# Kernel tuning notes

Hardware: AMD Instinct MI355X
Metric: run time of the kernel (lower is better)

## Reference

```python
import jax, jax.numpy as jnp
import numpy as np

NUM_WIRES = 12
NUM_LAYERS = 4
NUM_OUTPUTS = 4
BATCH = 1024
DIM = 2 ** NUM_WIRES


def _apply_1q(psi, U, w):
    # psi: (B, 2**n) complex64; U: (2,2) shared or (B,2,2) per-sample; wire 0 = most significant.
    B = psi.shape[0]
    L = 2 ** w
    R = DIM // (2 * L)
    psi = psi.reshape(B, L, 2, R)
    if U.ndim == 2:
        psi = jnp.einsum('ij,bljr->blir', U, psi)
    else:
        psi = jnp.einsum('bij,bljr->blir', U, psi)
    return psi.reshape(B, DIM)


def _cnot(psi, c, t):
    # CNOT(control=c, target=t): flip target amplitudes in the control=1 half.
    B = psi.shape[0]
    psi = psi.reshape((B,) + (2,) * NUM_WIRES)
    a0 = jax.lax.index_in_dim(psi, 0, c + 1, keepdims=True)
    a1 = jax.lax.index_in_dim(psi, 1, c + 1, keepdims=True)
    a1 = jnp.flip(a1, axis=t + 1)
    psi = jnp.concatenate([a0, a1], axis=c + 1)
    return psi.reshape(B, DIM)


def _rot(phi, theta, omega):
    # PennyLane Rot(phi, theta, omega) = RZ(omega) @ RY(theta) @ RZ(phi)
    c = jnp.cos(theta / 2)
    s = jnp.sin(theta / 2)
    u00 = jnp.exp(-0.5j * (phi + omega)) * c
    u01 = -jnp.exp(0.5j * (phi - omega)) * s
    u10 = jnp.exp(-0.5j * (phi - omega)) * s
    u11 = jnp.exp(0.5j * (phi + omega)) * c
    return jnp.stack([jnp.stack([u00, u01]), jnp.stack([u10, u11])]).astype(jnp.complex64)


def _circuit(inputs, weights):
    B = inputs.shape[0]
    psi = jnp.zeros((B, DIM), jnp.complex64).at[:, 0].set(1.0)
    # AngleEmbedding with rotation 'Y': RY(pi/2 * x_w) on wire w (per-sample angles)
    theta = (jnp.pi / 2) * inputs  # (B, n)
    c = jnp.cos(theta / 2)
    s = jnp.sin(theta / 2)
    for w in range(NUM_WIRES):
        U = jnp.stack([jnp.stack([c[:, w], -s[:, w]], -1),
                       jnp.stack([s[:, w], c[:, w]], -1)], -2).astype(jnp.complex64)  # (B,2,2)
        psi = _apply_1q(psi, U, w)
    # StronglyEntanglingLayers: Rot on every wire, then ring of CNOTs with range r
    for l in range(NUM_LAYERS):
        for w in range(NUM_WIRES):
            psi = _apply_1q(psi, _rot(weights[l, w, 0], weights[l, w, 1], weights[l, w, 2]), w)
        r = (l % (NUM_WIRES - 1)) + 1
        for w in range(NUM_WIRES):
            psi = _cnot(psi, w, (w + r) % NUM_WIRES)
    # expval(PauliZ) on the first NUM_OUTPUTS wires
    probs = jnp.abs(psi) ** 2  # (B, DIM) float32
    idx = jnp.arange(DIM)
    shifts = NUM_WIRES - 1 - jnp.arange(NUM_OUTPUTS)
    signs = (1.0 - 2.0 * ((idx[None, :] >> shifts[:, None]) & 1)).astype(probs.dtype)  # (NOUT, DIM)
    return probs @ signs.T  # (B, NUM_OUTPUTS)


def setup_inputs() -> dict:
    key = jax.random.key(0)
    k1, k2 = jax.random.split(key)
    inputs = jax.random.uniform(k1, (BATCH, NUM_WIRES), jnp.float32, -1.0, 1.0)
    weights = jax.random.uniform(k2, (NUM_LAYERS, NUM_WIRES, 3), jnp.float32, 0.0, 2.0 * np.pi)
    return {"inputs": inputs, "weights": weights}


def reference(inputs, weights):
    return _circuit(inputs, weights)
```

## Files before the change

### kernel.cpp

```cpp
#include <hip/hip_runtime.h>
#include <hip/hip_bf16.h>

#define NW 12
#define DIM 4096
#define NL 4
#define NGATE 48
#define NOUT 4
#define TPB 256

typedef float f32x2 __attribute__((ext_vector_type(2)));
typedef float f32x4 __attribute__((ext_vector_type(4)));
typedef unsigned u32x4 __attribute__((ext_vector_type(4)));
typedef short short8 __attribute__((ext_vector_type(8)));

constexpr int pcnt(unsigned x){ return __builtin_popcount(x); }
constexpr int msbp(unsigned x){ return x ? 31-__builtin_clz(x) : -1; }
constexpr unsigned ring_fwd(unsigned x,int r){
  for(int w=0;w<NW;++w){ int c=NW-1-w,t=NW-1-((w+r)%NW); x^=((x>>c)&1u)<<t; } return x;
}
constexpr unsigned ring_rev(unsigned x,int r){
  for(int w=NW-1;w>=0;--w){ int c=NW-1-w,t=NW-1-((w+r)%NW); x^=((x>>c)&1u)<<t; } return x;
}
struct Mat { unsigned col[12]; };
constexpr unsigned apply_cols(const Mat&M, unsigned v){
  unsigned r=0; for(int j=0;j<12;++j) if((v>>j)&1u) r^=M.col[j]; return r;
}
constexpr unsigned apply_rows(const unsigned* rows, unsigned v){
  unsigned r=0; for(int i=0;i<12;++i) r|=(unsigned)(pcnt(rows[i]&v)&1)<<i; return r;
}
constexpr bool invert_rows(const Mat&M, unsigned* ri_out){
  unsigned rb[12]={}, ri[12]={};
  for(int i=0;i<12;++i){ unsigned r=0; for(int j=0;j<12;++j) r|=((M.col[j]>>i)&1u)<<j; rb[i]=r; ri[i]=1u<<i; }
  for(int c=0;c<12;++c){
    int piv=-1; for(int r=c;r<12;++r) if((rb[r]>>c)&1u){piv=r;break;}
    if(piv<0) return false;
    unsigned t=rb[c]; rb[c]=rb[piv]; rb[piv]=t; t=ri[c]; ri[c]=ri[piv]; ri[piv]=t;
    for(int r=0;r<12;++r) if(r!=c&&((rb[r]>>c)&1u)){ rb[r]^=rb[c]; ri[r]^=ri[c]; }
  }
  for(int i=0;i<12;++i) ri_out[i]=ri[i];
  return true;
}
constexpr int nullspace4(const unsigned* A0, unsigned* out){
  unsigned A[4]={}; for(int i=0;i<4;++i) A[i]=A0[i];
  int rank=0; int pivc[4]={-1,-1,-1,-1};
  for(int c=0;c<12&&rank<4;++c){
    int piv=-1; for(int r=rank;r<4;++r) if((A[r]>>c)&1u){piv=r;break;}
    if(piv<0) continue;
    unsigned t=A[rank];A[rank]=A[piv];A[piv]=t;
    for(int r=0;r<4;++r) if(r!=rank&&((A[r]>>c)&1u)) A[r]^=A[rank];
    pivc[rank]=c; ++rank;
  }
  if(rank!=4) return -1;
  bool ispiv[12]={};
  for(int r=0;r<4;++r) ispiv[pivc[r]]=true;
  int cnt=0;
  for(int f=0;f<12;++f) if(!ispiv[f]){
    unsigned v=1u<<f;
    for(int r=0;r<4;++r) if((A[r]>>f)&1u) v|=1u<<pivc[r];
    out[cnt++]=v;
  }
  return cnt;
}
struct Ech { unsigned r[12]; int lead[12]; int n; };
constexpr unsigned ech_red(const Ech&e, unsigned v){
  int mv=msbp(v);
  for(int i=0;i<e.n&&v;++i) if(e.lead[i]==mv){ v^=e.r[i]; mv=msbp(v); }
  return v;
}
constexpr void ech_add(Ech&e, unsigned v){
  int l=msbp(v); int pos=e.n;
  while(pos>0&&e.lead[pos-1]<l){ e.r[pos]=e.r[pos-1]; e.lead[pos]=e.lead[pos-1]; --pos; }
  e.r[pos]=v; e.lead[pos]=l; e.n+=1;
}

struct Circ {
  unsigned M[NL][12]; unsigned RM[NL][12]; unsigned MR[NOUT];
};
constexpr Circ make_circ(){
  Circ C{};
  unsigned cols[12]={}, icols[12]={};
  for(int p=0;p<12;++p){ cols[p]=1u<<p; icols[p]=1u<<p; }
  for(int l=0;l<NL;++l){
    for(int w=0;w<NW;++w){
      int p=NW-1-w;
      C.M[l][w]=icols[p];
      unsigned r=0; for(int j=0;j<12;++j) r|=((cols[j]>>p)&1u)<<j;
      C.RM[l][w]=r;
    }
    int rr=(l%(NW-1))+1;
    for(int j=0;j<12;++j) cols[j]=ring_fwd(cols[j],rr);
    unsigned nic[12]={};
    for(int p=0;p<12;++p){
      unsigned y=ring_rev(1u<<p,rr), v=0;
      for(int q=0;q<12;++q) if((y>>q)&1u) v^=icols[q];
      nic[p]=v;
    }
    for(int p=0;p<12;++p) icols[p]=nic[p];
  }
  for(int o=0;o<NOUT;++o){
    int p=NW-1-o; unsigned r=0;
    for(int j=0;j<12;++j) r|=((cols[j]>>p)&1u)<<j;
    C.MR[o]=r;
  }
  return C;
}


constexpr unsigned amap(unsigned v){ return (v>>8)*2048u + (v&255u)*8u; }

struct Plan2 {
  unsigned SCOLt[8];
  unsigned SK16[16];
  unsigned TM;
  unsigned WBC[12][8], WOFF[12][16];
  unsigned RBC[12][8], ROFF[12][16];
  unsigned SRt[NOUT], KP[NOUT];
  bool ok;
};

constexpr Plan2 make_plan2(){
  Plan2 P{}; P.ok=true;
  constexpr Circ C = make_circ();
  const int SIGl[8] = {0,1,2,3,10,11,6,7};
  Mat Bprev{}; for(int j=0;j<12;++j) Bprev.col[j]=1u<<j;
  for(int g=0; g<12; ++g){
    int l=g/3, j0=(g%3)*4;
    unsigned mi[4]={}, rmi[4]={};
    for(int i=0;i<4;++i){ mi[i]=C.M[l][j0+i]; rmi[i]=C.RM[l][j0+i]; }
    unsigned u[8]={};
    if(nullspace4(rmi,u)!=8){ P.ok=false; return P; }
    unsigned binv[12]={};
    if(!invert_rows(Bprev,binv)){ P.ok=false; return P; }
    for(int s=0;s<8;++s) u[s]=apply_rows(binv,u[s]);
    Mat Bg{};
    for(int j=0;j<8;++j) Bg.col[j]=apply_cols(Bprev,u[j]);
    for(int i=0;i<4;++i) Bg.col[8+i]=mi[i];
    unsigned tinv[12]={};
    if(!invert_rows(Bg,tinv)){ P.ok=false; return P; }
    for(int i=0;i<4;++i)
      for(int j=0;j<12;++j){
        int want=(j==8+i)?1:0;
        if((pcnt(Bg.col[j]&rmi[i])&1)!=want){ P.ok=false; return P; }
      }
    if(g==0){
      for(int j=0;j<8;++j) P.SCOLt[j]=Bg.col[SIGl[j]];
      for(int idx=0;idx<16;++idx){
        unsigned v=0;
        if((idx>>2)&1) v^=Bg.col[4];
        if((idx>>2)&2) v^=Bg.col[5];
        if(idx&1) v^=Bg.col[8];
        if(idx&2) v^=Bg.col[9];
        P.SK16[idx]=v; P.TM|=v;
      }
    } else {
      unsigned rk[4]={};
      for(int i=0;i<4;++i){
        rk[i]=apply_rows(binv,mi[i]);
        if(apply_cols(Bprev,rk[i])!=mi[i]){ P.ok=false; return P; }
      }
      unsigned s2b[6]={u[0],u[1],u[2],u[3],rk[2],rk[3]};
      unsigned rows[12]={}; int nr=0;
      Ech P1{},P2{},ER{};
      for(int pick=0;pick<4;++pick){
        unsigned fx=0, fy=0;
        const int b1s[6]={0,1,2,3,10,11};
        for(int ii=0;ii<6;++ii){
          unsigned f=1u<<b1s[ii];
          unsigned p1=(f&15u)|(((f>>10)&3u)<<4);
          if(ech_red(P1,p1)){ fx=f; break; }
        }
        for(int bb=0;bb<12;++bb){
          unsigned f=1u<<bb, p2=0;
          for(int i2=0;i2<6;++i2) p2|=(unsigned)(pcnt(f&s2b[i2])&1)<<i2;
          if(ech_red(P2,p2)){ fy=f; break; }
        }
        if(!fx||!fy){ P.ok=false; return P; }
        unsigned cand[3]={fx,fy,fx^fy};
        unsigned chosen=0, cp1=0, cp2=0;
        for(int ci=0; ci<3 && !chosen; ++ci){
          unsigned f=cand[ci];
          unsigned p1=(f&15u)|(((f>>10)&3u)<<4);
          unsigned p2=0; for(int i2=0;i2<6;++i2) p2|=(unsigned)(pcnt(f&s2b[i2])&1)<<i2;
          if(ech_red(P1,p1)&&ech_red(P2,p2)){ chosen=f; cp1=p1; cp2=p2; }
        }
        if(!chosen){ P.ok=false; return P; }
        { unsigned v1=ech_red(P1,cp1); ech_add(P1,v1); }
        { unsigned v2=ech_red(P2,cp2); ech_add(P2,v2); }
        { unsigned vr=ech_red(ER,chosen); if(!vr){ P.ok=false; return P; } ech_add(ER,vr); }
        rows[nr++]=chosen;
      }
      for(int bb=0;bb<12 && nr<12;++bb){
        unsigned vr=ech_red(ER,1u<<bb); if(!vr) continue;
        ech_add(ER,vr); rows[nr++]=1u<<bb;
      }
      if(nr!=12){ P.ok=false; return P; }
      unsigned PhiCol[12]={};
      for(int j=0;j<12;++j){
        unsigned v=0;
        for(int i=0;i<12;++i) v|=(unsigned)((rows[i]>>j)&1u)<<i;
        PhiCol[j]=v;
      }
      unsigned PhiM[12]={};
      for(int j=0;j<12;++j){
        unsigned src=(j<8)? u[j] : rk[j-8];
        unsigned v=0;
        for(int q2=0;q2<12;++q2) if((src>>q2)&1u) v^=PhiCol[q2];
        PhiM[j]=v;
      }
      for(int j=0;j<8;++j){
        P.WBC[g][j]=amap(PhiCol[SIGl[j]]);
        P.RBC[g][j]=amap(PhiM[SIGl[j]]);
      }
      for(int idx=0;idx<16;++idx){
        unsigned wv=0, rv=0;
        if((idx>>2)&1){ wv^=PhiCol[4]; rv^=PhiM[4]; }
        if((idx>>2)&2){ wv^=PhiCol[5]; rv^=PhiM[5]; }
        if(idx&1){ wv^=PhiCol[8]; rv^=PhiM[8]; }
        if(idx&2){ wv^=PhiCol[9]; rv^=PhiM[9]; }
        P.WOFF[g][idx]=amap(wv); P.ROFF[g][idx]=amap(rv);
      }
    }
    Bprev=Bg;
  }
  for(int o=0;o<NOUT;++o){
    unsigned sr=0;
    for(int j=0;j<12;++j) sr|=(unsigned)(pcnt(Bprev.col[j]&C.MR[o])&1)<<j;
    unsigned srt=0;
    const int SIGl2[8] = {0,1,2,3,10,11,6,7};
    for(int j=0;j<8;++j) srt|=((sr>>SIGl2[j])&1u)<<j;
    P.SRt[o]=srt;
    unsigned kp=0;
    for(int idx=0;idx<16;++idx){
      int T=idx>>2, q=idx&3;
      unsigned bit=(((sr>>4)&1u)&(unsigned)(T&1))^(((sr>>5)&1u)&(unsigned)((T>>1)&1))
                  ^(((sr>>8)&1u)&(unsigned)(q&1))^(((sr>>9)&1u)&(unsigned)((q>>1)&1));
      kp|=bit<<idx;
    }
    P.KP[o]=kp;
  }
  return P;
}

constexpr Plan2 PL2C = make_plan2();
static_assert(PL2C.ok, "plan2 failed");
__device__ constexpr Plan2 PL2 = PL2C;

struct Plan {
  unsigned SCOL0[8]; unsigned SK16_0[16];
  unsigned WTC[12][8]; unsigned WK16[12][16];
  unsigned RDC[12][8]; unsigned WRK16[12][16];
  unsigned SRlow[NOUT], SRhigh[NOUT];
  unsigned TM; bool ok;
};
constexpr Plan make_plan(){
  Plan P{}; P.ok=true;
  constexpr Circ C = make_circ();
  Mat Bprev{}; for(int j=0;j<12;++j) Bprev.col[j]=1u<<j;
  for(int g=0; g<12; ++g){
    int l=g/3, j0=(g%3)*4;
    unsigned mi[4]={}, rmi[4]={};
    for(int i=0;i<4;++i){ mi[i]=C.M[l][j0+i]; rmi[i]=C.RM[l][j0+i]; }
    unsigned u[8]={};
    if(nullspace4(rmi,u)!=8){ P.ok=false; return P; }
    unsigned binv[12]={};
    if(!invert_rows(Bprev,binv)){ P.ok=false; return P; }
    for(int s=0;s<8;++s) u[s]=apply_rows(binv,u[s]);
    Mat Bg{};
    for(int j=0;j<8;++j) Bg.col[j]=apply_cols(Bprev,u[j]);
    for(int i=0;i<4;++i) Bg.col[8+i]=mi[i];
    unsigned tinv[12]={};
    if(!invert_rows(Bg,tinv)){ P.ok=false; return P; }
    for(int i=0;i<4;++i)
      for(int j=0;j<12;++j){
        int want=(j==8+i)?1:0;
        if((pcnt(Bg.col[j]&rmi[i])&1)!=want){ P.ok=false; return P; }
      }
    if(g==0){
      for(int j=0;j<8;++j) P.SCOL0[j]=Bg.col[j];
      unsigned tm=0;
      for(int k=0;k<16;++k){
        unsigned v=0; for(int i=0;i<4;++i) if((k>>i)&1) v^=Bg.col[8+i];
        P.SK16_0[k]=v; tm|=v;
      }
      P.TM=tm;
    } else {
      unsigned rk[4]={};
      for(int i=0;i<4;++i){
        rk[i]=apply_rows(binv,mi[i]);
        if(apply_cols(Bprev,rk[i])!=mi[i]){ P.ok=false; return P; }
      }
      unsigned row2[12]={};
      for(int bb=0;bb<12;++bb){
        unsigned r=0;
        for(int j=0;j<6;++j) r |= ((u[j]>>bb)&1u) << j;
        row2[bb]=r;
      }
      unsigned rows[12]={}; int nr=0;
      Ech P1{}; Ech P2{}; Ech ER{};
      for(int pick=0;pick<4;++pick){
        int b1=-1;
        for(int bb=0;bb<6;++bb){ if(ech_red(P1, 1u<<bb)){ b1=bb; break; } }
        int b2=-1;
        for(int bb=0;bb<12;++bb){ if(ech_red(P2, row2[bb])){ b2=bb; break; } }
        if(b1<0||b2<0){ P.ok=false; return P; }
        unsigned p2x=row2[b1];
        unsigned p1y=(b2<6)?(1u<<b2):0u;
        unsigned f=0, p1f=0, p2f=0;
        if(ech_red(P2,p2x))      { f=1u<<b1;            p1f=1u<<b1;          p2f=p2x; }
        else if(ech_red(P1,p1y)) { f=1u<<b2;            p1f=p1y;             p2f=row2[b2]; }
        else                     { f=(1u<<b1)^(1u<<b2); p1f=(1u<<b1)^p1y;    p2f=p2x^row2[b2]; }
        unsigned v1=ech_red(P1,p1f), v2=ech_red(P2,p2f);
        if(!v1||!v2){ P.ok=false; return P; }
        ech_add(P1,v1); ech_add(P2,v2);
        unsigned vr=ech_red(ER,f);
        if(!vr){ P.ok=false; return P; }
        ech_add(ER,vr);
        rows[nr++]=f;
      }
      for(int bb=0;bb<12 && nr<12;++bb){
        unsigned vr=ech_red(ER,1u<<bb); if(!vr) continue;
        ech_add(ER,vr); rows[nr++]=1u<<bb;
      }
      if(nr!=12){ P.ok=false; return P; }
      unsigned Wcol[12]={};
      for(int j=0;j<12;++j){
        unsigned v=0;
        for(int i=0;i<12;++i) v |= ((rows[i]>>j)&1u)<<i;
        Wcol[j]=v;
      }
      for(int j=0;j<8;++j){
        P.WTC[g][j]=Wcol[j];
        unsigned v=0;
        for(int q=0;q<12;++q) if((u[j]>>q)&1u) v^=Wcol[q];
        P.RDC[g][j]=v;
      }
      for(int k=0;k<16;++k){
        unsigned wv=0, rv=0;
        for(int i=0;i<4;++i) if((k>>i)&1){
          wv ^= Wcol[8+i];
          unsigned v=0;
          for(int q=0;q<12;++q) if((rk[i]>>q)&1u) v^=Wcol[q];
          rv ^= v;
        }
        P.WK16[g][k]=wv; P.WRK16[g][k]=rv;
      }
    }
    Bprev=Bg;
  }
  for(int o=0;o<NOUT;++o){
    unsigned sr=0;
    for(int j=0;j<12;++j) sr|=(unsigned)(pcnt(Bprev.col[j]&C.MR[o])&1)<<j;
    P.SRlow[o]=sr&255u; P.SRhigh[o]=sr>>8;
  }
  return P;
}
constexpr Plan PLC = make_plan();
static_assert(PLC.ok, "plan1 failed");
__device__ constexpr Plan PL = PLC;

__device__ __forceinline__ void gate_coeffs(const float* __restrict__ wts, int gi, float* o){
  const float* w = wts + gi*3;
  float st,ct;  sincosf(0.5f*w[1],&st,&ct);
  float sap,cap; sincosf(0.5f*(w[0]+w[2]),&sap,&cap);
  float sam,cam; sincosf(0.5f*(w[0]-w[2]),&sam,&cam);
  o[0]= cap*ct; o[1]=-sap*ct;
  o[2]=-cam*st; o[3]=-sam*st;
  o[4]= cam*st; o[5]=-sam*st;
  o[6]= cap*ct; o[7]= sap*ct;
}
__device__ __forceinline__ unsigned cvtpk(float a, float b){
  unsigned r; asm("v_cvt_pk_bf16_f32 %0, %1, %2" : "=v"(r) : "v"(a), "v"(b)); return r;
}
__device__ __forceinline__ void split2(float x, float& hf, float& lf){
  __hip_bfloat16 hb = __float2bfloat16(x);
  hf = __bfloat162float(hb);
  lf = x - hf;
}

__global__ void coeff2_kernel(const float* __restrict__ wts, unsigned short* __restrict__ gfrag){
  const int g = blockIdx.x;
  const int tid = threadIdx.x;
  const int m = tid & 15, rp = tid >> 4;
  const int s = rp >> 1, reg = rp & 1;
  const int r0 = 4*s + 2*reg, r1 = r0 + 1;
  const int l = g/3, j0 = (g%3)*4;
  float ur0=1.f, ui0=0.f, ur1=1.f, ui1=0.f;
  #pragma unroll
  for(int i=0;i<4;++i){
    float o[8]; gate_coeffs(wts, l*NW + j0 + i, o);
    int mb=(m>>i)&1, rb0=(r0>>i)&1, rb1=(r1>>i)&1;
    float er=o[(mb*2+rb0)*2], ei=o[(mb*2+rb0)*2+1];
    float tr=ur0*er-ui0*ei, ti=ur0*ei+ui0*er; ur0=tr; ui0=ti;
    er=o[(mb*2+rb1)*2]; ei=o[(mb*2+rb1)*2+1];
    tr=ur1*er-ui1*ei; ti=ur1*ei+ui1*er; ur1=tr; ui1=ti;
  }
  float ur0h,ur0l,ur1h,ur1l, ui0h,ui0l,ui1h,ui1l;
  split2(ur0,ur0h,ur0l); split2(ur1,ur1h,ur1l);
  split2(ui0,ui0h,ui0l); split2(ui1,ui1h,ui1l);
  unsigned Urh=cvtpk(ur0h,ur1h), Url=cvtpk(ur0l,ur1l);
  unsigned Uih=cvtpk(ui0h,ui1h), Uil=cvtpk(ui0l,ui1l);
  unsigned nUih=Uih^0x80008000u, nUil=Uil^0x80008000u;
  const int lane = s*16 + m;
  unsigned p0[6]={Urh,Url,Uih,Uil,nUih,nUil};
  unsigned p1[6]={Url,Urh,Uil,Uih,nUil,nUih};
  #pragma unroll
  for(int f=0; f<6; ++f){
    unsigned* fp = (unsigned*)((char*)gfrag + ((size_t)((g*6+f)*64 + lane))*16);
    fp[reg] = p0[f];
    fp[2+reg] = p1[f];
  }
}

__global__ __launch_bounds__(TPB,4)
void vqc_mfma(const float* __restrict__ inp, const unsigned short* __restrict__ gfrag,
              float* __restrict__ out){
  __shared__ __align__(16) char smem[DIM*8];
  float* cs = (float*)smem; float* ss = cs+NW; float* red = cs+2*NW;
  char* ampc = smem;
  const int t = threadIdx.x, b = blockIdx.x, l = t&63;
  if(t < NW){
    float x = inp[b*NW+t];
    float s,c; sincosf(0.78539816339744830962f*x,&s,&c);
    cs[t]=c; ss[t]=s;
  }
  __syncthreads();
  float ctm[12], stm[12];
  #pragma unroll
  for(int p=0;p<12;++p){ ctm[p]=cs[11-p]; stm[p]=ss[11-p]; }
  unsigned sigb=0;
  #pragma unroll
  for(int j=0;j<8;++j) sigb ^= ((t>>j)&1u)? PL2.SCOLt[j] : 0u;
  float pbase=1.f;
  #pragma unroll
  for(int p=0;p<12;++p)
    if(!((PL2C.TM>>p)&1u))
      pbase *= ((sigb>>p)&1u)? stm[p] : ctm[p];

  f32x4 Cr[4], Ci[4];
  #pragma unroll 1
  for(int g=0; g<12; ++g){
    if(g>0){
      unsigned wbase=0;
      #pragma unroll
      for(int j=0;j<8;++j) wbase ^= ((t>>j)&1u)? PL2.WBC[g][j] : 0u;
      __syncthreads();
      #pragma unroll
      for(int idx=0; idx<16; ++idx){
        const int T=idx>>2, q=idx&3;
        *(float2*)(ampc + (wbase ^ PL2.WOFF[g][idx])) = make_float2(Cr[T][q], Ci[T][q]);
      }
      __syncthreads();
    }
    short8 AF[6];
    #pragma unroll
    for(int f=0; f<6; ++f)
      AF[f] = *(const short8*)((const char*)gfrag + ((size_t)((g*6+f)*64 + l))*16);
    unsigned rbase=0;
    if(g>0){
      #pragma unroll
      for(int j=0;j<8;++j) rbase ^= ((t>>j)&1u)? PL2.RBC[g][j] : 0u;
    }
    #pragma unroll
    for(int T=0;T<4;++T){
      float2 v0,v1,v2,v3;
      if(g==0){
        float vv[4];
        #pragma unroll
        for(int rq=0;rq<4;++rq){
          unsigned sig = sigb ^ PL2.SK16[T*4+rq];
          float pk=pbase;
          #pragma unroll
          for(int p=0;p<12;++p)
            if((PL2C.TM>>p)&1u)
              pk *= ((sig>>p)&1u)? stm[p] : ctm[p];
          vv[rq]=pk;
        }
        v0=make_float2(vv[0],0.f); v1=make_float2(vv[1],0.f);
        v2=make_float2(vv[2],0.f); v3=make_float2(vv[3],0.f);
      } else {
        v0 = *(const float2*)(ampc + (rbase ^ PL2.ROFF[g][T*4+0]));
        v1 = *(const float2*)(ampc + (rbase ^ PL2.ROFF[g][T*4+1]));
        v2 = *(const float2*)(ampc + (rbase ^ PL2.ROFF[g][T*4+2]));
        v3 = *(const float2*)(ampc + (rbase ^ PL2.ROFF[g][T*4+3]));
      }
      float h0,h1,h2,h3,e0,e1,e2,e3;
      split2(v0.x,h0,e0); split2(v1.x,h1,e1); split2(v2.x,h2,e2); split2(v3.x,h3,e3);
      u32x4 bu; bu.x=cvtpk(h0,h1); bu.y=cvtpk(h2,h3); bu.z=cvtpk(e0,e1); bu.w=cvtpk(e2,e3);
      short8 Br = __builtin_bit_cast(short8, bu);
      split2(v0.y,h0,e0); split2(v1.y,h1,e1); split2(v2.y,h2,e2); split2(v3.y,h3,e3);
      u32x4 cu; cu.x=cvtpk(h0,h1); cu.y=cvtpk(h2,h3); cu.z=cvtpk(e0,e1); cu.w=cvtpk(e2,e3);
      short8 Bi = __builtin_bit_cast(short8, cu);
      const f32x4 z = {0.f,0.f,0.f,0.f};
      f32x4 cr = __builtin_amdgcn_mfma_f32_16x16x32_bf16(AF[0], Br, z, 0,0,0);
      cr = __builtin_amdgcn_mfma_f32_16x16x32_bf16(AF[1], Br, cr, 0,0,0);
      cr = __builtin_amdgcn_mfma_f32_16x16x32_bf16(AF[4], Bi, cr, 0,0,0);
      cr = __builtin_amdgcn_mfma_f32_16x16x32_bf16(AF[5], Bi, cr, 0,0,0);
      f32x4 ci = __builtin_amdgcn_mfma_f32_16x16x32_bf16(AF[2], Br, z, 0,0,0);
      ci = __builtin_amdgcn_mfma_f32_16x16x32_bf16(AF[3], Br, ci, 0,0,0);
      ci = __builtin_amdgcn_mfma_f32_16x16x32_bf16(AF[0], Bi, ci, 0,0,0);
      ci = __builtin_amdgcn_mfma_f32_16x16x32_bf16(AF[1], Bi, ci, 0,0,0);
      Cr[T]=cr; Ci[T]=ci;
    }
  }
  float acc[NOUT]={0.f,0.f,0.f,0.f};
  float sg[NOUT];
  #pragma unroll
  for(int o=0;o<NOUT;++o)
    sg[o] = (__popc((unsigned)t & PL2.SRt[o])&1)? -1.f : 1.f;
  #pragma unroll
  for(int idx=0; idx<16; ++idx){
    const int T=idx>>2, q=idx&3;
    float pr = Cr[T][q]*Cr[T][q] + Ci[T][q]*Ci[T][q];
    #pragma unroll
    for(int o=0;o<NOUT;++o){
      const bool kp = (PL2C.KP[o]>>idx)&1;
      float f = sg[o]*pr;
      acc[o] += kp? -f : f;
    }
  }
  #pragma unroll
  for(int o=0;o<NOUT;++o)
    #pragma unroll
    for(int off=32; off>0; off>>=1)
      acc[o] += __shfl_down(acc[o], off);
  __syncthreads();
  const int wv=t>>6, ln=t&63;
  if(ln==0){
    #pragma unroll
    for(int o=0;o<NOUT;++o) red[wv*NOUT+o]=acc[o];
  }
  __syncthreads();
  if(t<NOUT)
    out[b*NOUT+t] = red[0*NOUT+t]+red[1*NOUT+t]+red[2*NOUT+t]+red[3*NOUT+t];
}

__global__ __launch_bounds__(TPB,4)
void vqc_fb(const float* __restrict__ inp, const float* __restrict__ wts,
            float* __restrict__ out){
  __shared__ __align__(16) char smem[DIM*8 + NGATE*8*4];
  f32x2* amp = (f32x2*)smem;
  float* cs  = (float*)smem;
  float* ss  = cs + NW;
  float* red = cs + 2*NW;
  float* gtab = (float*)(smem + DIM*8);
  const int t = threadIdx.x;
  const int b = blockIdx.x;
  if(t < NW){
    float x = inp[b*NW+t];
    float s,c; sincosf(0.78539816339744830962f*x,&s,&c);
    cs[t]=c; ss[t]=s;
  }
  if(t < NGATE){
    float o[8]; gate_coeffs(wts,t,o);
    #pragma unroll
    for(int j=0;j<8;++j) gtab[t*8+j]=o[j];
  }
  __syncthreads();
  float cr[NW], sr_[NW];
  #pragma unroll
  for(int w=0;w<NW;++w){ cr[w]=cs[w]; sr_[w]=ss[w]; }
  unsigned sig_t=0;
  #pragma unroll
  for(int j=0;j<8;++j) sig_t ^= ((t>>j)&1u)? PL.SCOL0[j] : 0u;
  float pbase=1.f;
  #pragma unroll
  for(int p=0;p<12;++p)
    if(!((PLC.TM>>p)&1u))
      pbase *= ((sig_t>>p)&1u)? sr_[11-p] : cr[11-p];
  f32x2 a[16];
  #pragma unroll
  for(int k=0;k<16;++k){
    float pk=pbase;
    #pragma unroll
    for(int p=0;p<12;++p)
      if((PLC.TM>>p)&1u){
        unsigned bit = ((sig_t ^ PL.SK16_0[k])>>p)&1u;
        pk *= bit? sr_[11-p] : cr[11-p];
      }
    a[k].x=pk; a[k].y=0.f;
  }
  const float* gw = (const float*)gtab;
  #pragma unroll 1
  for(int g=0; g<12; ++g){
    if(g>0){
      unsigned wb=0, rb=0;
      #pragma unroll
      for(int j=0;j<8;++j){
        wb ^= ((t>>j)&1u)? PL.WTC[g][j] : 0u;
        rb ^= ((t>>j)&1u)? PL.RDC[g][j] : 0u;
      }
      __syncthreads();
      #pragma unroll
      for(int k=0;k<16;++k) amp[wb ^ PL.WK16[g][k]] = a[k];
      __syncthreads();
      #pragma unroll
      for(int k=0;k<16;++k) a[k] = amp[rb ^ PL.WRK16[g][k]];
    }
    #pragma unroll
    for(int i=0;i<4;++i){
      const float* w = gw + (g*4+i)*8;
      f32x2 c00={w[0],w[0]}, d00={-w[1],w[1]};
      f32x2 c01={w[2],w[2]}, d01={-w[3],w[3]};
      f32x2 c10={w[4],w[4]}, d10={-w[5],w[5]};
      f32x2 c11={w[6],w[6]}, d11={-w[7],w[7]};
      #pragma unroll
      for(int q=0;q<8;++q){
        const int k0=((q>>i)<<(i+1))|(q&((1<<i)-1));
        const int k1=k0|(1<<i);
        f32x2 a0=a[k0], a1=a[k1];
        f32x2 a0s=a0.yx, a1s=a1.yx;
        f32x2 n0 = c00*a0 + d00*a0s + c01*a1 + d01*a1s;
        f32x2 n1 = c10*a0 + d10*a0s + c11*a1 + d11*a1s;
        a[k0]=n0; a[k1]=n1;
      }
    }
  }
  float acc[NOUT]={0.f,0.f,0.f,0.f};
  float sg[NOUT];
  #pragma unroll
  for(int o=0;o<NOUT;++o)
    sg[o] = (__popc((unsigned)t & PL.SRlow[o])&1)? -1.f : 1.f;
  #pragma unroll
  for(int k=0;k<16;++k){
    float pr = a[k].x*a[k].x + a[k].y*a[k].y;
    #pragma unroll
    for(int o=0;o<NOUT;++o){
      const bool kp = (PLC.SRhigh[o]>>0 ? ((pcnt((unsigned)k & PLC.SRhigh[o])&1)!=0) : false);
      float f = sg[o]*pr;
      acc[o] += kp ? -f : f;
    }
  }
  #pragma unroll
  for(int o=0;o<NOUT;++o)
    #pragma unroll
    for(int off=32; off>0; off>>=1)
      acc[o] += __shfl_down(acc[o], off);
  __syncthreads();
  const int wv=t>>6, ln=t&63;
  if(ln==0){
    #pragma unroll
    for(int o=0;o<NOUT;++o) red[wv*NOUT+o]=acc[o];
  }
  __syncthreads();
  if(t<NOUT)
    out[b*NOUT+t] = red[0*NOUT+t]+red[1*NOUT+t]+red[2*NOUT+t]+red[3*NOUT+t];
}

extern "C" void kernel_launch(void* const* d_in, const int* in_sizes, int n_in,
                              void* d_out, int out_size, void* d_ws, size_t ws_size,
                              hipStream_t stream) {
  const float* inp=(const float*)d_in[0];
  const float* wts=(const float*)d_in[1];
  float* outp=(float*)d_out;
  const int B = in_sizes[0]/NW;
  const size_t FRAG_BYTES = (size_t)12*6*64*16;
  if(ws_size >= FRAG_BYTES){
    unsigned short* gfrag=(unsigned short*)d_ws;
    coeff2_kernel<<<12,128,0,stream>>>(wts,gfrag);
    vqc_mfma<<<B,TPB,0,stream>>>(inp,gfrag,outp);
  } else {
    vqc_fb<<<B,TPB,0,stream>>>(inp,wts,outp);
  }
}
```

Measured before the change: 44.28 us.

## Prefetch gate fragments, use LDS LUT for base offsets, cheaper bf16 split

```diff
diff --git a/kernel.cpp b/kernel.cpp
--- a/kernel.cpp
+++ b/kernel.cpp
@@ -104,7 +104,6 @@
   }
   return C;
 }
-
 
 constexpr unsigned amap(unsigned v){ return (v>>8)*2048u + (v&255u)*8u; }
 
@@ -376,6 +375,13 @@
   hf = __bfloat162float(hb);
   lf = x - hf;
 }
+__device__ __forceinline__ void pkhl(float x0, float x1, unsigned& hw_out, unsigned& lw_out){
+  unsigned hw = cvtpk(x0, x1);
+  float h0 = __uint_as_float(hw << 16);
+  float h1 = __uint_as_float(hw & 0xffff0000u);
+  lw_out = cvtpk(x0 - h0, x1 - h1);
+  hw_out = hw;
+}
 
 __global__ void coeff2_kernel(const float* __restrict__ wts, unsigned short* __restrict__ gfrag){
   const int g = blockIdx.x;
@@ -411,18 +417,33 @@
   }
 }
 
+#define LUT_BYTES (11*64*4)
 __global__ __launch_bounds__(TPB,4)
 void vqc_mfma(const float* __restrict__ inp, const unsigned short* __restrict__ gfrag,
               float* __restrict__ out){
-  __shared__ __align__(16) char smem[DIM*8];
+  __shared__ __align__(16) char smem[DIM*8 + LUT_BYTES];
   float* cs = (float*)smem; float* ss = cs+NW; float* red = cs+2*NW;
   char* ampc = smem;
+  unsigned* blut = (unsigned*)(smem + DIM*8);
   const int t = threadIdx.x, b = blockIdx.x, l = t&63;
   if(t < NW){
     float x = inp[b*NW+t];
     float s,c; sincosf(0.78539816339744830962f*x,&s,&c);
     cs[t]=c; ss[t]=s;
   }
+  for(int e=t; e<11*64; e+=TPB){
+    int gg=(e>>6)+1, idx=e&63;
+    int kind=idx>>4, nib=idx&15;
+    unsigned v=0;
+    #pragma unroll
+    for(int j=0;j<4;++j){
+      if((nib>>j)&1){
+        int jj = j + ((kind&1)?4:0);
+        v ^= (kind<2)? PL2.WBC[gg][jj] : PL2.RBC[gg][jj];
+      }
+    }
+    blut[e]=v;
+  }
   __syncthreads();
   float ctm[12], stm[12];
   #pragma unroll
@@ -436,13 +457,19 @@
     if(!((PL2C.TM>>p)&1u))
       pbase *= ((sigb>>p)&1u)? stm[p] : ctm[p];
 
+  short8 AF[6];
+  #pragma unroll
+  for(int f=0; f<6; ++f)
+    AF[f] = *(const short8*)((const char*)gfrag + ((size_t)(f*64 + l))*16);
+
   f32x4 Cr[4], Ci[4];
   #pragma unroll 1
   for(int g=0; g<12; ++g){
+    unsigned rbase=0;
     if(g>0){
-      unsigned wbase=0;
-      #pragma unroll
-      for(int j=0;j<8;++j) wbase ^= ((t>>j)&1u)? PL2.WBC[g][j] : 0u;
+      const unsigned* bl = blut + (g-1)*64;
+      unsigned wbase = bl[t&15] ^ bl[16 + (t>>4)];
+      rbase          = bl[32 + (t&15)] ^ bl[48 + (t>>4)];
       __syncthreads();
       #pragma unroll
       for(int idx=0; idx<16; ++idx){
@@ -450,15 +477,6 @@
         *(float2*)(ampc + (wbase ^ PL2.WOFF[g][idx])) = make_float2(Cr[T][q], Ci[T][q]);
       }
       __syncthreads();
-    }
-    short8 AF[6];
-    #pragma unroll
-    for(int f=0; f<6; ++f)
-      AF[f] = *(const short8*)((const char*)gfrag + ((size_t)((g*6+f)*64 + l))*16);
-    unsigned rbase=0;
-    if(g>0){
-      #pragma unroll
-      for(int j=0;j<8;++j) rbase ^= ((t>>j)&1u)? PL2.RBC[g][j] : 0u;
     }
     #pragma unroll
     for(int T=0;T<4;++T){
@@ -483,12 +501,14 @@
         v2 = *(const float2*)(ampc + (rbase ^ PL2.ROFF[g][T*4+2]));
         v3 = *(const float2*)(ampc + (rbase ^ PL2.ROFF[g][T*4+3]));
       }
-      float h0,h1,h2,h3,e0,e1,e2,e3;
-      split2(v0.x,h0,e0); split2(v1.x,h1,e1); split2(v2.x,h2,e2); split2(v3.x,h3,e3);
-      u32x4 bu; bu.x=cvtpk(h0,h1); bu.y=cvtpk(h2,h3); bu.z=cvtpk(e0,e1); bu.w=cvtpk(e2,e3);
+      unsigned h0,l0,h1,l1;
+      pkhl(v0.x, v1.x, h0, l0);
+      pkhl(v2.x, v3.x, h1, l1);
+      u32x4 bu; bu.x=h0; bu.y=h1; bu.z=l0; bu.w=l1;
       short8 Br = __builtin_bit_cast(short8, bu);
-      split2(v0.y,h0,e0); split2(v1.y,h1,e1); split2(v2.y,h2,e2); split2(v3.y,h3,e3);
-      u32x4 cu; cu.x=cvtpk(h0,h1); cu.y=cvtpk(h2,h3); cu.z=cvtpk(e0,e1); cu.w=cvtpk(e2,e3);
+      pkhl(v0.y, v1.y, h0, l0);
+      pkhl(v2.y, v3.y, h1, l1);
+      u32x4 cu; cu.x=h0; cu.y=h1; cu.z=l0; cu.w=l1;
       short8 Bi = __builtin_bit_cast(short8, cu);
       const f32x4 z = {0.f,0.f,0.f,0.f};
       f32x4 cr = __builtin_amdgcn_mfma_f32_16x16x32_bf16(AF[0], Br, z, 0,0,0);
@@ -500,6 +520,11 @@
       ci = __builtin_amdgcn_mfma_f32_16x16x32_bf16(AF[0], Bi, ci, 0,0,0);
       ci = __builtin_amdgcn_mfma_f32_16x16x32_bf16(AF[1], Bi, ci, 0,0,0);
       Cr[T]=cr; Ci[T]=ci;
+    }
+    if(g<11){
+      #pragma unroll
+      for(int f=0; f<6; ++f)
+        AF[f] = *(const short8*)((const char*)gfrag + ((size_t)(((g+1)*6+f)*64 + l))*16);
     }
   }
   float acc[NOUT]={0.f,0.f,0.f,0.f};
@@ -625,7 +650,7 @@
     float pr = a[k].x*a[k].x + a[k].y*a[k].y;
     #pragma unroll
     for(int o=0;o<NOUT;++o){
-      const bool kp = (PLC.SRhigh[o]>>0 ? ((pcnt((unsigned)k & PLC.SRhigh[o])&1)!=0) : false);
+      const bool kp = (pcnt((unsigned)k & PLC.SRhigh[o])&1)!=0;
       float f = sg[o]*pr;
       acc[o] += kp ? -f : f;
     }
```

Measured after the change: 40.78 us. -7.9%, faster.
